# Kernel optimization log

Hardware: AMD Instinct MI355X
Metric: run time of the kernel (lower is better)

## Reference

```python
import jax, jax.numpy as jnp
import numpy as np

B, C, H, W = 16, 512, 64, 64   # C == e_dim
N_E = 256                       # codebook size
BETA = 0.25


def setup_inputs() -> dict:
    key = jax.random.key(0)
    k1, k2, k3 = jax.random.split(key, 3)
    z = jax.random.normal(k1, (B, C, H, W), dtype=jnp.float32)
    # nn.Embedding init: uniform(-1/n_e, 1/n_e)
    emb_weight = jax.random.uniform(k2, (N_E, C), dtype=jnp.float32,
                                    minval=-1.0 / N_E, maxval=1.0 / N_E)
    std_param = jnp.array(1.0, dtype=jnp.float32)
    means = jnp.zeros((3,), dtype=jnp.float32)
    conv_w = jax.random.normal(k3, (C, C), dtype=jnp.float32) * 0.02  # 1x1 conv kernel [out,in]
    conv_b = jnp.zeros((C,), dtype=jnp.float32)
    return {"z": z, "emb_weight": emb_weight, "std_param": std_param,
            "means": means, "conv_w": conv_w, "conv_b": conv_b}


def reference(z, emb_weight, std_param, means, conv_w, conv_b):
    # torch uses .item() on std/mean -> detached scalars
    std = jax.lax.stop_gradient(jnp.abs(std_param))
    mean = jax.lax.stop_gradient(jnp.mean(means))
    w = emb_weight * std + mean                      # [n_e, C] scaled codebook

    zf = z.transpose(0, 2, 3, 1).reshape(-1, C)       # [N, C], N = B*H*W
    # pairwise squared L2: ||z||^2 + ||w||^2 - 2 z.w
    d = (jnp.sum(zf * zf, axis=1, keepdims=True)
         + jnp.sum(w * w, axis=1)
         - 2.0 * zf @ w.T)                            # [N, n_e]
    idx = jnp.argmin(d, axis=1)                       # [N]
    one_hot = jax.nn.one_hot(idx, N_E, dtype=z.dtype) # [N, n_e]

    z_q = (one_hot @ w).reshape(B, H, W, C).transpose(0, 3, 1, 2)  # [B,C,H,W]

    sg = jax.lax.stop_gradient
    loss = jnp.mean((sg(z_q) - z) ** 2) + BETA * jnp.mean((z_q - sg(z)) ** 2)

    z_q = z + sg(z_q - z)                             # straight-through

    e_mean = jnp.mean(one_hot, axis=0)                # [n_e]
    perplexity = jnp.exp(-jnp.sum(e_mean * jnp.log(e_mean + 1e-10)))

    # 1x1 conv == channel matmul
    out = jnp.einsum('bchw,oc->bohw', z_q, conv_w) + conv_b[None, :, None, None]
    return out, loss, perplexity
```

## Files before the change

### kernel.cpp

```cpp
#include <hip/hip_runtime.h>


#define C_DIM 512
#define N_E   256
#define HW    4096
#define SAr   72

typedef unsigned short u16;
typedef u16   u16x4 __attribute__((ext_vector_type(4)));
typedef u16   u16x8 __attribute__((ext_vector_type(8)));
typedef short s16x8 __attribute__((ext_vector_type(8)));
typedef float f32x4 __attribute__((ext_vector_type(4)));

__device__ __forceinline__ u16 f2bf(float f) {
    unsigned u = __float_as_uint(f);
    return (u16)((u + 0x7FFFu + ((u >> 16) & 1u)) >> 16);
}

__global__ __launch_bounds__(256)
void prep(const float* __restrict__ emb, const float* __restrict__ stdp,
          const float* __restrict__ means, const float* __restrict__ convw,
          const float* __restrict__ convb,
          u16* __restrict__ wfrag, float* __restrict__ wnorm,
          float* __restrict__ M2T, float* __restrict__ accum,
          unsigned int* __restrict__ hist) {
    int t = threadIdx.x;
    float stdv  = fabsf(stdp[0]);
    float meanv = (means[0] + means[1] + means[2]) * (1.0f / 3.0f);

    if (blockIdx.x < 256) {
        int c = blockIdx.x;
        if (c == 0) {
            hist[t] = 0u;
            if (t < 2) accum[t] = 0.f;
        }
        float ss = 0.f;
        for (int k = t; k < C_DIM; k += 256) {
            float w = emb[c * C_DIM + k] * stdv + meanv;
            ss += w * w;
            int ntg  = c >> 4;
            int lane = (c & 15) | (((k >> 3) & 3) << 4);
            int ksg  = k >> 5;
            int j    = k & 7;
            wfrag[((ntg * 16 + ksg) * 64 + lane) * 8 + j] = f2bf(w);
        }
        #pragma unroll
        for (int m = 1; m < 64; m <<= 1) ss += __shfl_xor(ss, m, 64);
        __shared__ float red[4];
        if ((t & 63) == 0) red[t >> 6] = ss;
        __syncthreads();
        if (t == 0) wnorm[c] = red[0] + red[1] + red[2] + red[3];
    } else {
        __shared__ float cw[4][C_DIM];
        int o0 = (blockIdx.x - 256) * 4;
        for (int i = t; i < 4 * C_DIM; i += 256)
            cw[i >> 9][i & 511] = convw[(o0 + (i >> 9)) * C_DIM + (i & 511)];
        __syncthreads();
        float a0 = 0.f, a1 = 0.f, a2 = 0.f, a3 = 0.f;
        const float* er = emb + t * C_DIM;
        #pragma unroll 4
        for (int k = 0; k < C_DIM; k += 4) {
            f32x4 ev = *(const f32x4*)(er + k);
            #pragma unroll
            for (int jj = 0; jj < 4; ++jj) {
                float w = ev[jj] * stdv + meanv;
                a0 += cw[0][k + jj] * w;
                a1 += cw[1][k + jj] * w;
                a2 += cw[2][k + jj] * w;
                a3 += cw[3][k + jj] * w;
            }
        }
        M2T[(o0 + 0) * N_E + t] = a0 + convb[o0 + 0];
        M2T[(o0 + 1) * N_E + t] = a1 + convb[o0 + 1];
        M2T[(o0 + 2) * N_E + t] = a2 + convb[o0 + 2];
        M2T[(o0 + 3) * N_E + t] = a3 + convb[o0 + 3];
    }
}

__global__ __launch_bounds__(256, 2)
void argmin_out(const float* __restrict__ z, const u16* __restrict__ wfrag,
                const float* __restrict__ wnorm, const float* __restrict__ M2T,
                float* __restrict__ out,
                float* __restrict__ accum, unsigned int* __restrict__ hist) {
    __shared__ u16 Ab[2][128 * SAr];
    __shared__ unsigned long long lmin[128];
    __shared__ unsigned int lhist[N_E];
    __shared__ float lred[8];
    __shared__ u16 lcode[128];

    int tid = threadIdx.x;
    int wave = tid >> 6, lane = tid & 63;
    int mhalf = wave & 1, nhalf = wave >> 1;
    int bb = blockIdx.x;
    const float* zb = z + (size_t)(bb >> 5) * (C_DIM * HW) + (bb & 31) * 128;

    if (tid < 128) lmin[tid] = ~0ull;
    lhist[tid] = 0u;

    f32x4 acc[4][8];
    #pragma unroll
    for (int mt = 0; mt < 4; ++mt)
        #pragma unroll
        for (int nt = 0; nt < 8; ++nt)
            acc[mt][nt] = (f32x4){0.f, 0.f, 0.f, 0.f};

    int t5 = tid & 31, cg = tid >> 5;
    const float* gsrc = zb + (size_t)(cg * 8) * HW + t5 * 4;
    int skey = (t5 >> 1) & 7;
    int wch  = (cg * 8) ^ (skey * 8);
    float zs = 0.f;

    int m15 = lane & 15, quad = lane >> 4;
    const u16x8* wf8 = (const u16x8*)wfrag;

    f32x4 sv[8];
    #pragma unroll
    for (int i = 0; i < 8; ++i) sv[i] = *(const f32x4*)(gsrc + (size_t)i * HW);
    #pragma unroll
    for (int p = 0; p < 4; ++p) {
        u16x8 pk;
        #pragma unroll
        for (int i = 0; i < 8; ++i) { float f = sv[i][p]; zs += f * f; pk[i] = f2bf(f); }
        *(u16x8*)(&Ab[0][(t5 * 4 + p) * SAr + wch]) = pk;
    }

    for (int kc = 0; kc < 8; ++kc) {
        int cur = kc & 1;
        if (kc < 7) {
            const float* g2 = gsrc + (size_t)((kc + 1) * 64) * HW;
            #pragma unroll
            for (int i = 0; i < 8; ++i) sv[i] = *(const f32x4*)(g2 + (size_t)i * HW);
        }
        __syncthreads();
        #pragma unroll
        for (int ks = 0; ks < 2; ++ks) {
            s16x8 bfr[8];
            #pragma unroll
            for (int nt = 0; nt < 8; ++nt) {
                int ntg = nhalf * 8 + nt, ksg = kc * 2 + ks;
                bfr[nt] = __builtin_bit_cast(s16x8, wf8[(ntg * 16 + ksg) * 64 + lane]);
            }
            s16x8 am[4];
            #pragma unroll
            for (int mt = 0; mt < 4; ++mt) {
                int pos = mhalf * 64 + mt * 16 + m15;
                int rkey = (mt * 2 + (m15 >> 3)) & 7;
                int rch = (ks * 32 + quad * 8) ^ (rkey * 8);
                am[mt] = __builtin_bit_cast(s16x8, *(const u16x8*)(&Ab[cur][pos * SAr + rch]));
            }
            #pragma unroll
            for (int mt = 0; mt < 4; ++mt)
                #pragma unroll
                for (int nt = 0; nt < 8; ++nt)
                    acc[mt][nt] = __builtin_amdgcn_mfma_f32_16x16x32_bf16(
                        am[mt], bfr[nt], acc[mt][nt], 0, 0, 0);
        }
        if (kc < 7) {
            #pragma unroll
            for (int p = 0; p < 4; ++p) {
                u16x8 pk;
                #pragma unroll
                for (int i = 0; i < 8; ++i) { float f = sv[i][p]; zs += f * f; pk[i] = f2bf(f); }
                *(u16x8*)(&Ab[cur ^ 1][(t5 * 4 + p) * SAr + wch]) = pk;
            }
        }
    }

    float wn[8];
    #pragma unroll
    for (int nt = 0; nt < 8; ++nt) wn[nt] = wnorm[(nhalf * 8 + nt) * 16 + m15];

    #pragma unroll
    for (int mt = 0; mt < 4; ++mt) {
        #pragma unroll
        for (int r = 0; r < 4; ++r) {
            unsigned long long key = ~0ull;
            #pragma unroll
            for (int nt = 0; nt < 8; ++nt) {
                float d = wn[nt] - 2.0f * acc[mt][nt][r];
                unsigned u = __float_as_uint(d);
                u ^= (u >> 31) ? 0xFFFFFFFFu : 0x80000000u;
                unsigned code = (unsigned)((nhalf * 8 + nt) * 16 + m15);
                unsigned long long k2 = ((unsigned long long)u << 32) | code;
                key = (k2 < key) ? k2 : key;
            }
            #pragma unroll
            for (int sm = 1; sm < 16; sm <<= 1) {
                unsigned long long o2 = (unsigned long long)__shfl_xor((long long)key, sm, 64);
                key = (o2 < key) ? o2 : key;
            }
            if (m15 == 0) {
                int pos = mhalf * 64 + mt * 16 + quad * 4 + r;
                atomicMin(&lmin[pos], key);
            }
        }
    }
    __syncthreads();

    float dsum = 0.f;
    if (tid < 128) {
        unsigned long long key = lmin[tid];
        unsigned code = (unsigned)(key & 0xFFFFu);
        unsigned u = (unsigned)(key >> 32);
        u ^= (u >> 31) ? 0x80000000u : 0xFFFFFFFFu;
        dsum = __uint_as_float(u);
        lcode[tid] = (u16)code;
        atomicAdd(&lhist[code], 1u);
    }
    #pragma unroll
    for (int sm = 1; sm < 64; sm <<= 1) {
        dsum += __shfl_xor(dsum, sm, 64);
        zs   += __shfl_xor(zs, sm, 64);
    }
    if (lane == 0) { lred[wave] = dsum; lred[4 + wave] = zs; }
    __syncthreads();
    if (tid == 0) {
        atomicAdd(&accum[0], lred[4] + lred[5] + lred[6] + lred[7]);
        atomicAdd(&accum[1], lred[0] + lred[1] + lred[2] + lred[3]);
    }
    unsigned cnt = lhist[tid];
    if (cnt) atomicAdd(&hist[tid], cnt);

    int t5o = tid & 31, oo = tid >> 5;
    int ec[4];
    #pragma unroll
    for (int jj = 0; jj < 4; ++jj) ec[jj] = (int)lcode[t5o * 4 + jj];
    float* obase = out + ((size_t)(bb >> 5) * C_DIM + oo) * HW + (bb & 31) * 128 + t5o * 4;
    const float* m2 = M2T + oo * N_E;
    #pragma unroll 4
    for (int og = 0; og < C_DIM; og += 8) {
        f32x4 r;
        #pragma unroll
        for (int jj = 0; jj < 4; ++jj) r[jj] = m2[og * N_E + ec[jj]];
        *(f32x4*)(obase + (size_t)og * HW) = r;
    }
}

__global__ __launch_bounds__(256)
void fin_k(const float* __restrict__ accum, const unsigned int* __restrict__ hist,
           float* __restrict__ out) {
    int tid = threadIdx.x;
    float e = (float)hist[tid] * (1.0f / 65536.0f);
    float term = e * logf(e + 1e-10f);
    #pragma unroll
    for (int m = 1; m < 64; m <<= 1) term += __shfl_xor(term, m, 64);
    __shared__ float red[4];
    if ((tid & 63) == 0) red[tid >> 6] = term;
    __syncthreads();
    if (tid == 0) {
        float s = red[0] + red[1] + red[2] + red[3];
        out[33554432] = 1.25f * (accum[0] + accum[1]) * (1.0f / 33554432.0f);
        out[33554433] = expf(-s);
    }
}

extern "C" void kernel_launch(void* const* d_in, const int* in_sizes, int n_in,
                              void* d_out, int out_size, void* d_ws, size_t ws_size,
                              hipStream_t stream) {
    (void)in_sizes; (void)n_in; (void)out_size; (void)ws_size;
    const float* z     = (const float*)d_in[0];
    const float* emb   = (const float*)d_in[1];
    const float* stdp  = (const float*)d_in[2];
    const float* means = (const float*)d_in[3];
    const float* convw = (const float*)d_in[4];
    const float* convb = (const float*)d_in[5];

    char* ws = (char*)d_ws;
    u16*   wfrag = (u16*)(ws + 0);
    float* wnorm = (float*)(ws + 262144);
    float* M2T   = (float*)(ws + 263168);
    float* accum = (float*)(ws + 787456);
    unsigned int* hist = (unsigned int*)(ws + 787464);
    float* out = (float*)d_out;

    prep      <<<384, 256, 0, stream>>>(emb, stdp, means, convw, convb,
                                        wfrag, wnorm, M2T, accum, hist);
    argmin_out<<<512, 256, 0, stream>>>(z, wfrag, wnorm, M2T, out, accum, hist);
    fin_k     <<<1,   256, 0, stream>>>(accum, hist, out);
}
```

Baseline: 301.8 us.

## Halve argmin block tile to 64 rows, split codebook across 4 waves

The argmin/output kernel now processes 64 spatial positions per block instead of 128, launching 1024 blocks. Each of the 4 waves covers a quarter of the codebook for all 64 rows, which halves the accumulator registers and LDS use and allows 4 blocks per CU. The aim is more parallelism and occupancy to hide the memory-bound z loads and output stores. The cost is that every codebook fragment is read from global/L2 by twice as many blocks, and the block now reuses each B fragment only across 4 M tiles.

```diff
diff --git a/kernel.cpp b/kernel.cpp
--- a/kernel.cpp
+++ b/kernel.cpp
@@ -77,51 +77,51 @@
     }
 }
 
-__global__ __launch_bounds__(256, 2)
+__global__ __launch_bounds__(256, 4)
 void argmin_out(const float* __restrict__ z, const u16* __restrict__ wfrag,
                 const float* __restrict__ wnorm, const float* __restrict__ M2T,
                 float* __restrict__ out,
                 float* __restrict__ accum, unsigned int* __restrict__ hist) {
-    __shared__ u16 Ab[2][128 * SAr];
-    __shared__ unsigned long long lmin[128];
+    __shared__ u16 Ab[2][64 * SAr];
+    __shared__ unsigned long long lmin[64];
     __shared__ unsigned int lhist[N_E];
     __shared__ float lred[8];
-    __shared__ u16 lcode[128];
+    __shared__ u16 lcode[64];
 
     int tid = threadIdx.x;
     int wave = tid >> 6, lane = tid & 63;
-    int mhalf = wave & 1, nhalf = wave >> 1;
+    int nq = wave;
     int bb = blockIdx.x;
-    const float* zb = z + (size_t)(bb >> 5) * (C_DIM * HW) + (bb & 31) * 128;
-
-    if (tid < 128) lmin[tid] = ~0ull;
+    const float* zb = z + (size_t)(bb >> 6) * (C_DIM * HW) + (bb & 63) * 64;
+
+    if (tid < 64) lmin[tid] = ~0ull;
     lhist[tid] = 0u;
 
-    f32x4 acc[4][8];
+    f32x4 acc[4][4];
     #pragma unroll
     for (int mt = 0; mt < 4; ++mt)
         #pragma unroll
-        for (int nt = 0; nt < 8; ++nt)
+        for (int nt = 0; nt < 4; ++nt)
             acc[mt][nt] = (f32x4){0.f, 0.f, 0.f, 0.f};
 
-    int t5 = tid & 31, cg = tid >> 5;
-    const float* gsrc = zb + (size_t)(cg * 8) * HW + t5 * 4;
-    int skey = (t5 >> 1) & 7;
-    int wch  = (cg * 8) ^ (skey * 8);
+    int t4 = tid & 15, cg = tid >> 4;
+    const float* gsrc = zb + (size_t)(cg * 4) * HW + t4 * 4;
+    int skey = (t4 >> 1) & 7;
+    int wch  = (((cg >> 1) ^ skey) * 8) + ((cg & 1) * 4);
     float zs = 0.f;
 
     int m15 = lane & 15, quad = lane >> 4;
     const u16x8* wf8 = (const u16x8*)wfrag;
 
-    f32x4 sv[8];
-    #pragma unroll
-    for (int i = 0; i < 8; ++i) sv[i] = *(const f32x4*)(gsrc + (size_t)i * HW);
+    f32x4 sv[4];
+    #pragma unroll
+    for (int i = 0; i < 4; ++i) sv[i] = *(const f32x4*)(gsrc + (size_t)i * HW);
     #pragma unroll
     for (int p = 0; p < 4; ++p) {
-        u16x8 pk;
-        #pragma unroll
-        for (int i = 0; i < 8; ++i) { float f = sv[i][p]; zs += f * f; pk[i] = f2bf(f); }
-        *(u16x8*)(&Ab[0][(t5 * 4 + p) * SAr + wch]) = pk;
+        u16x4 pk;
+        #pragma unroll
+        for (int i = 0; i < 4; ++i) { float f = sv[i][p]; zs += f * f; pk[i] = f2bf(f); }
+        *(u16x4*)(&Ab[0][(t4 * 4 + p) * SAr + wch]) = pk;
     }
 
     for (int kc = 0; kc < 8; ++kc) {
@@ -129,46 +129,43 @@
         if (kc < 7) {
             const float* g2 = gsrc + (size_t)((kc + 1) * 64) * HW;
             #pragma unroll
-            for (int i = 0; i < 8; ++i) sv[i] = *(const f32x4*)(g2 + (size_t)i * HW);
+            for (int i = 0; i < 4; ++i) sv[i] = *(const f32x4*)(g2 + (size_t)i * HW);
         }
         __syncthreads();
         #pragma unroll
         for (int ks = 0; ks < 2; ++ks) {
-            s16x8 bfr[8];
-            #pragma unroll
-            for (int nt = 0; nt < 8; ++nt) {
-                int ntg = nhalf * 8 + nt, ksg = kc * 2 + ks;
-                bfr[nt] = __builtin_bit_cast(s16x8, wf8[(ntg * 16 + ksg) * 64 + lane]);
-            }
             s16x8 am[4];
             #pragma unroll
             for (int mt = 0; mt < 4; ++mt) {
-                int pos = mhalf * 64 + mt * 16 + m15;
                 int rkey = (mt * 2 + (m15 >> 3)) & 7;
                 int rch = (ks * 32 + quad * 8) ^ (rkey * 8);
-                am[mt] = __builtin_bit_cast(s16x8, *(const u16x8*)(&Ab[cur][pos * SAr + rch]));
-            }
-            #pragma unroll
-            for (int mt = 0; mt < 4; ++mt)
+                am[mt] = __builtin_bit_cast(s16x8,
+                    *(const u16x8*)(&Ab[cur][(mt * 16 + m15) * SAr + rch]));
+            }
+            #pragma unroll
+            for (int nt = 0; nt < 4; ++nt) {
+                int ntg = nq * 4 + nt, ksg = kc * 2 + ks;
+                s16x8 bfr = __builtin_bit_cast(s16x8, wf8[(ntg * 16 + ksg) * 64 + lane]);
                 #pragma unroll
-                for (int nt = 0; nt < 8; ++nt)
+                for (int mt = 0; mt < 4; ++mt)
                     acc[mt][nt] = __builtin_amdgcn_mfma_f32_16x16x32_bf16(
-                        am[mt], bfr[nt], acc[mt][nt], 0, 0, 0);
+                        am[mt], bfr, acc[mt][nt], 0, 0, 0);
+            }
         }
         if (kc < 7) {
             #pragma unroll
             for (int p = 0; p < 4; ++p) {
-                u16x8 pk;
+                u16x4 pk;
                 #pragma unroll
-                for (int i = 0; i < 8; ++i) { float f = sv[i][p]; zs += f * f; pk[i] = f2bf(f); }
-                *(u16x8*)(&Ab[cur ^ 1][(t5 * 4 + p) * SAr + wch]) = pk;
-            }
-        }
-    }
-
-    float wn[8];
-    #pragma unroll
-    for (int nt = 0; nt < 8; ++nt) wn[nt] = wnorm[(nhalf * 8 + nt) * 16 + m15];
+                for (int i = 0; i < 4; ++i) { float f = sv[i][p]; zs += f * f; pk[i] = f2bf(f); }
+                *(u16x4*)(&Ab[cur ^ 1][(t4 * 4 + p) * SAr + wch]) = pk;
+            }
+        }
+    }
+
+    float wn[4];
+    #pragma unroll
+    for (int nt = 0; nt < 4; ++nt) wn[nt] = wnorm[(nq * 4 + nt) * 16 + m15];
 
     #pragma unroll
     for (int mt = 0; mt < 4; ++mt) {
@@ -176,11 +173,11 @@
         for (int r = 0; r < 4; ++r) {
             unsigned long long key = ~0ull;
             #pragma unroll
-            for (int nt = 0; nt < 8; ++nt) {
+            for (int nt = 0; nt < 4; ++nt) {
                 float d = wn[nt] - 2.0f * acc[mt][nt][r];
                 unsigned u = __float_as_uint(d);
                 u ^= (u >> 31) ? 0xFFFFFFFFu : 0x80000000u;
-                unsigned code = (unsigned)((nhalf * 8 + nt) * 16 + m15);
+                unsigned code = (unsigned)((nq * 4 + nt) * 16 + m15);
                 unsigned long long k2 = ((unsigned long long)u << 32) | code;
                 key = (k2 < key) ? k2 : key;
             }
@@ -190,7 +187,7 @@
                 key = (o2 < key) ? o2 : key;
             }
             if (m15 == 0) {
-                int pos = mhalf * 64 + mt * 16 + quad * 4 + r;
+                int pos = mt * 16 + quad * 4 + r;
                 atomicMin(&lmin[pos], key);
             }
         }
@@ -198,7 +195,7 @@
     __syncthreads();
 
     float dsum = 0.f;
-    if (tid < 128) {
+    if (tid < 64) {
         unsigned long long key = lmin[tid];
         unsigned code = (unsigned)(key & 0xFFFFu);
         unsigned u = (unsigned)(key >> 32);
@@ -216,19 +213,19 @@
     __syncthreads();
     if (tid == 0) {
         atomicAdd(&accum[0], lred[4] + lred[5] + lred[6] + lred[7]);
-        atomicAdd(&accum[1], lred[0] + lred[1] + lred[2] + lred[3]);
+        atomicAdd(&accum[1], lred[0]);
     }
     unsigned cnt = lhist[tid];
     if (cnt) atomicAdd(&hist[tid], cnt);
 
-    int t5o = tid & 31, oo = tid >> 5;
+    int t4o = tid & 15, oo = tid >> 4;
     int ec[4];
     #pragma unroll
-    for (int jj = 0; jj < 4; ++jj) ec[jj] = (int)lcode[t5o * 4 + jj];
-    float* obase = out + ((size_t)(bb >> 5) * C_DIM + oo) * HW + (bb & 31) * 128 + t5o * 4;
+    for (int jj = 0; jj < 4; ++jj) ec[jj] = (int)lcode[t4o * 4 + jj];
+    float* obase = out + ((size_t)(bb >> 6) * C_DIM + oo) * HW + (bb & 63) * 64 + t4o * 4;
     const float* m2 = M2T + oo * N_E;
     #pragma unroll 4
-    for (int og = 0; og < C_DIM; og += 8) {
+    for (int og = 0; og < C_DIM; og += 16) {
         f32x4 r;
         #pragma unroll
         for (int jj = 0; jj < 4; ++jj) r[jj] = m2[og * N_E + ec[jj]];
@@ -273,8 +270,8 @@
     unsigned int* hist = (unsigned int*)(ws + 787464);
     float* out = (float*)d_out;
 
-    prep      <<<384, 256, 0, stream>>>(emb, stdp, means, convw, convb,
-                                        wfrag, wnorm, M2T, accum, hist);
-    argmin_out<<<512, 256, 0, stream>>>(z, wfrag, wnorm, M2T, out, accum, hist);
-    fin_k     <<<1,   256, 0, stream>>>(accum, hist, out);
-}
+    prep      <<<384,  256, 0, stream>>>(emb, stdp, means, convw, convb,
+                                         wfrag, wnorm, M2T, accum, hist);
+    argmin_out<<<1024, 256, 0, stream>>>(z, wfrag, wnorm, M2T, out, accum, hist);
+    fin_k     <<<1,    256, 0, stream>>>(accum, hist, out);
+}
```

Measured after the change: 325.7 us. 7.9% more time.
